# Optimization experiments

Measured on AMD Instinct MI355X. Metric: run time of the kernel, lower is better.

## Reference

```python
import jax, jax.numpy as jnp
import numpy as np

B, C, H, W = 16, 512, 64, 64
K = 32


def setup_inputs() -> dict:
    key = jax.random.key(0)
    k1, k2, k3 = jax.random.split(key, 3)
    std = 1.0 / (64 * C) ** 0.5
    x = jax.random.normal(k1, (B, C, H, W), dtype=jnp.float32)
    codewords = jax.random.uniform(k2, (K, C), dtype=jnp.float32, minval=-std, maxval=std)
    scale = jax.random.uniform(k3, (K,), dtype=jnp.float32, minval=-1.0, maxval=0.0)
    return {"x": x, "codewords": codewords, "scale": scale}


def reference(x, codewords, scale):
    b, c, h, w = x.shape
    # (b, n, c) with n = h*w spatial positions
    xf = x.reshape(b, c, h * w).transpose(0, 2, 1)
    x2 = jnp.sum(xf * xf, axis=-1)                       # (b, n)
    c2 = jnp.sum(codewords * codewords, axis=-1)          # (k,)
    xc = jnp.einsum('bnc,kc->bnk', xf, codewords)         # (b, n, k)
    logits = scale[None, None, :] * (x2[:, :, None] - 2.0 * xc + c2[None, None, :])
    A = jax.nn.softmax(logits, axis=2)                    # (b, n, k)
    # sum_n A[b,n,k] * (x[b,n,c] - codewords[k,c])
    encoded = jnp.einsum('bnk,bnc->bkc', A, xf) - jnp.einsum('bnk,kc->bkc', A, codewords)
    return encoded
```

## Files before the change

### kernel.cpp

```cpp
#include <hip/hip_runtime.h>
#include <hip/hip_bf16.h>
#include <math.h>

#define BB 16
#define CC 512
#define NN 4096
#define KK 32

typedef __attribute__((ext_vector_type(8))) short short8;
typedef __attribute__((ext_vector_type(4))) short short4v;
typedef __attribute__((ext_vector_type(4))) float float4v;

static __device__ __forceinline__ unsigned short f2bf(float f) {
  unsigned u = __float_as_uint(f);
  u += 0x7FFF + ((u >> 16) & 1);
  return (unsigned short)(u >> 16);
}

static __device__ __forceinline__ short8 cat8(short4v a, short4v b) {
  short8 r;
  r[0] = a[0]; r[1] = a[1]; r[2] = a[2]; r[3] = a[3];
  r[4] = b[0]; r[5] = b[1]; r[6] = b[2]; r[7] = b[3];
  return r;
}


__global__ __launch_bounds__(256) void prep_kernel(
    const float* __restrict__ cw, unsigned short* __restrict__ cwP,
    float* __restrict__ c2, float* __restrict__ asum) {
  int gid = blockIdx.x * 256 + threadIdx.x;
  if (gid < BB * KK) asum[gid] = 0.f;
  {
    int k = gid >> 9;
    int cc = gid & 511;
    int cs = cc & ~31;
    int w5 = cc & 31;
    int q = w5 >> 3, j = w5 & 7;
    int src_c = cs + 2 * q + (j & 1) + ((j >> 1) << 3);
    cwP[gid] = f2bf(cw[k * CC + src_c]);
  }
  __shared__ float c2p[KK][8];
  if (blockIdx.x == 0) {
    int k = threadIdx.x >> 3, j = threadIdx.x & 7;
    const float* row = cw + k * CC + j * 64;
    float s = 0.f;
    for (int i = 0; i < 64; ++i) s = fmaf(row[i], row[i], s);
    c2p[k][j] = s;
    __syncthreads();
    if (threadIdx.x < KK) {
      float t = 0.f;
      for (int j2 = 0; j2 < 8; ++j2) t += c2p[threadIdx.x][j2];
      c2[threadIdx.x] = t;
    }
  }
}

#define XP2 36
template <int LOG2CH>
__global__ __launch_bounds__(256, 4) void fused_kernel(
    const float* __restrict__ x, const unsigned short* __restrict__ cwP,
    const float* __restrict__ c2g, const float* __restrict__ scale,
    float* __restrict__ partials, float* __restrict__ asum) {
  constexpr int CHN = NN >> LOG2CH;
  constexpr int SUBS = CHN / 32;
  const int b = blockIdx.x >> LOG2CH;
  const int chunk = blockIdx.x & ((1 << LOG2CH) - 1);
  const int t = threadIdx.x;
  const int w = t >> 6;
  const int l = t & 63;
  const int l15 = l & 15;
  const int q = l >> 4;
  const int wrole = (w + (blockIdx.x & 3)) & 3;

  __shared__ unsigned short Xl[CC * XP2];
  __shared__ unsigned short As[KK * XP2];
  __shared__ float Sx2w[4 * 32];
  __shared__ float Sx2[32];

  const float* xb0 = x + (size_t)b * CC * NN + chunk * CHN;

  const float sc0 = scale[l15], sc1 = scale[16 + l15];
  const float cc0 = c2g[l15], cc1 = c2g[16 + l15];

  float4v acc[8][2];
#pragma unroll
  for (int ct = 0; ct < 8; ++ct)
#pragma unroll
    for (int m = 0; m < 2; ++m) acc[ct][m] = (float4v){0.f, 0.f, 0.f, 0.f};
  float s0acc = 0.f, s1acc = 0.f;

  const int f4 = t & 7;
  const int cr = t >> 3;

  for (int sub = 0; sub < SUBS; ++sub) {
    const float* xb = xb0 + sub * 32;

    float4v x2p = (float4v){0.f, 0.f, 0.f, 0.f};
#pragma unroll 8
    for (int i = 0; i < 16; ++i) {
      const int c = cr + 32 * i;
      float4v v = *(const float4v*)(xb + (size_t)c * NN + 4 * f4);
      x2p.x = fmaf(v.x, v.x, x2p.x);
      x2p.y = fmaf(v.y, v.y, x2p.y);
      x2p.z = fmaf(v.z, v.z, x2p.z);
      x2p.w = fmaf(v.w, v.w, x2p.w);
      unsigned p0 = (unsigned)f2bf(v.x) | ((unsigned)f2bf(v.y) << 16);
      unsigned p1 = (unsigned)f2bf(v.z) | ((unsigned)f2bf(v.w) << 16);
      *(uint2*)&Xl[c * XP2 + 4 * f4] = make_uint2(p0, p1);
    }
#pragma unroll
    for (int m = 8; m <= 32; m <<= 1) {
      x2p.x += __shfl_xor(x2p.x, m);
      x2p.y += __shfl_xor(x2p.y, m);
      x2p.z += __shfl_xor(x2p.z, m);
      x2p.w += __shfl_xor(x2p.w, m);
    }
    if (l < 8) *(float4v*)&Sx2w[w * 32 + 4 * l] = x2p;
    __syncthreads();

    float4v p0 = (float4v){0.f, 0.f, 0.f, 0.f};
    float4v p1 = (float4v){0.f, 0.f, 0.f, 0.f};
    if (wrole < 2) {
      const int nrow = wrole * 16 + l15;
      for (int cs = 0; cs < 512; cs += 32) {
        const int cb2 = cs + 2 * q;
        short8 af;
#pragma unroll
        for (int j = 0; j < 8; ++j) {
          const int c = cb2 + (j & 1) + ((j >> 1) << 3);
          af[j] = (short)Xl[c * XP2 + nrow];
        }
        short8 b0 = *(const short8*)(cwP + (size_t)l15 * CC + cs + q * 8);
        short8 b1 = *(const short8*)(cwP + (size_t)(16 + l15) * CC + cs + q * 8);
        p0 = __builtin_amdgcn_mfma_f32_16x16x32_bf16(af, b0, p0, 0, 0, 0);
        p1 = __builtin_amdgcn_mfma_f32_16x16x32_bf16(af, b1, p1, 0, 0, 0);
      }
    } else if (wrole == 2 && l < 32) {
      Sx2[l] = Sx2w[l] + Sx2w[32 + l] + Sx2w[64 + l] + Sx2w[96 + l];
    }
    __syncthreads();

    if (wrole < 2) {
      float a0[4], a1[4];
#pragma unroll
      for (int r = 0; r < 4; ++r) {
        const float xx = Sx2[wrole * 16 + 4 * q + r];
        float l0 = sc0 * (xx - 2.f * p0[r] + cc0);
        float l1 = sc1 * (xx - 2.f * p1[r] + cc1);
        float m = fmaxf(l0, l1);
        m = fmaxf(m, __shfl_xor(m, 1));
        m = fmaxf(m, __shfl_xor(m, 2));
        m = fmaxf(m, __shfl_xor(m, 4));
        m = fmaxf(m, __shfl_xor(m, 8));
        float e0 = __expf(l0 - m), e1 = __expf(l1 - m);
        float s = e0 + e1;
        s += __shfl_xor(s, 1);
        s += __shfl_xor(s, 2);
        s += __shfl_xor(s, 4);
        s += __shfl_xor(s, 8);
        float inv = 1.0f / s;
        a0[r] = e0 * inv;
        a1[r] = e1 * inv;
      }
      s0acc += a0[0] + a0[1] + a0[2] + a0[3];
      s1acc += a1[0] + a1[1] + a1[2] + a1[3];
      unsigned p00 = (unsigned)f2bf(a0[0]) | ((unsigned)f2bf(a0[1]) << 16);
      unsigned p01 = (unsigned)f2bf(a0[2]) | ((unsigned)f2bf(a0[3]) << 16);
      unsigned p10 = (unsigned)f2bf(a1[0]) | ((unsigned)f2bf(a1[1]) << 16);
      unsigned p11 = (unsigned)f2bf(a1[2]) | ((unsigned)f2bf(a1[3]) << 16);
      const int nc = wrole * 16 + 4 * q;
      *(uint2*)&As[l15 * XP2 + nc] = make_uint2(p00, p01);
      *(uint2*)&As[(16 + l15) * XP2 + nc] = make_uint2(p10, p11);
    }
    __syncthreads();

    {
      const int nb = q * 8;
      const short4v* Ap0 = (const short4v*)&As[l15 * XP2 + nb];
      const short4v* Ap1 = (const short4v*)&As[(16 + l15) * XP2 + nb];
      short8 am0 = cat8(Ap0[0], Ap0[1]);
      short8 am1 = cat8(Ap1[0], Ap1[1]);
#pragma unroll
      for (int ct = 0; ct < 8; ++ct) {
        const int c = w * 128 + ct * 16 + l15;
        const short4v* Bp = (const short4v*)&Xl[c * XP2 + nb];
        short8 bx = cat8(Bp[0], Bp[1]);
        acc[ct][0] = __builtin_amdgcn_mfma_f32_16x16x32_bf16(am0, bx, acc[ct][0], 0, 0, 0);
        acc[ct][1] = __builtin_amdgcn_mfma_f32_16x16x32_bf16(am1, bx, acc[ct][1], 0, 0, 0);
      }
    }
    __syncthreads();
  }

  float* pout = partials + (size_t)blockIdx.x * KK * CC;
#pragma unroll
  for (int ct = 0; ct < 8; ++ct) {
    const int c = w * 128 + ct * 16 + l15;
#pragma unroll
    for (int m = 0; m < 2; ++m)
#pragma unroll
      for (int r = 0; r < 4; ++r) {
        int k = 16 * m + 4 * q + r;
        pout[k * CC + c] = acc[ct][m][r];
      }
  }
  s0acc += __shfl_xor(s0acc, 16);
  s0acc += __shfl_xor(s0acc, 32);
  s1acc += __shfl_xor(s1acc, 16);
  s1acc += __shfl_xor(s1acc, 32);
  if (wrole < 2 && q == 0) {
    atomicAdd(&asum[b * KK + l15], s0acc);
    atomicAdd(&asum[b * KK + 16 + l15], s1acc);
  }
}

template <int LOG2CH>
__global__ __launch_bounds__(256) void reduce_kernel(
    const float* __restrict__ partials, const float* __restrict__ asum,
    const float* __restrict__ cw, float* __restrict__ out) {
  constexpr int P = 1 << LOG2CH;
  int idx = blockIdx.x * 256 + threadIdx.x;
  int b = idx >> 12;
  int k = (idx >> 7) & 31;
  int c4 = idx & 127;

  float4v o = {0.f, 0.f, 0.f, 0.f};
  const float4v* pb =
      (const float4v*)partials + (((size_t)b << LOG2CH) * KK + k) * 128 + c4;
#pragma unroll 8
  for (int p = 0; p < P; ++p) {
    float4v v = pb[(size_t)p * KK * 128];
    o.x += v.x;
    o.y += v.y;
    o.z += v.z;
    o.w += v.w;
  }
  float4v wv = ((const float4v*)cw)[k * 128 + c4];
  float a = asum[b * KK + k];
  o.x -= a * wv.x;
  o.y -= a * wv.y;
  o.z -= a * wv.z;
  o.w -= a * wv.w;
  ((float4v*)out)[idx] = o;
}

extern "C" void kernel_launch(void* const* d_in, const int* in_sizes, int n_in,
                              void* d_out, int out_size, void* d_ws, size_t ws_size,
                              hipStream_t stream) {
  const float* x = (const float*)d_in[0];
  const float* cw = (const float*)d_in[1];
  const float* scale = (const float*)d_in[2];
  float* out = (float*)d_out;
  char* ws = (char*)d_ws;

  float* c2 = (float*)ws;
  unsigned short* cwP = (unsigned short*)(ws + 128);
  float* asum = (float*)(ws + 32896);
  float* partials = (float*)(ws + 35072);

  prep_kernel<<<64, 256, 0, stream>>>(cw, cwP, c2, asum);

  const size_t need1024 = 35072 + (size_t)1024 * KK * CC * sizeof(float);
  if (ws_size >= need1024) {
    fused_kernel<6><<<1024, 256, 0, stream>>>(x, cwP, c2, scale, partials, asum);
    reduce_kernel<6><<<256, 256, 0, stream>>>(partials, asum, cw, out);
  } else {
    fused_kernel<5><<<512, 256, 0, stream>>>(x, cwP, c2, scale, partials, asum);
    reduce_kernel<5><<<256, 256, 0, stream>>>(partials, asum, cw, out);
  }
}
```

Before: 226.3 us.

## Prefetch next x sub-tile into registers and use LDS-only barriers

Software-pipelines the global loads of x: the first half of the next sub-tile's channels is loaded into registers while the current sub-tile's GEMM and softmax stages run, and the second half is issued at the start of each iteration. __syncthreads is replaced with a custom barrier that only waits on LDS counters, so outstanding global prefetch loads are not drained at each barrier. This hides HBM latency at the cost of extra VGPRs (two arrays of 8 float4s), which may lower occupancy.

Measured after the change: 272.8 us. 20.5% more time.

```diff
diff --git a/kernel.cpp b/kernel.cpp
--- a/kernel.cpp
+++ b/kernel.cpp
@@ -22,6 +22,11 @@
   r[0] = a[0]; r[1] = a[1]; r[2] = a[2]; r[3] = a[3];
   r[4] = b[0]; r[5] = b[1]; r[6] = b[2]; r[7] = b[3];
   return r;
+}
+
+static __device__ __forceinline__ void bar_lds() {
+  asm volatile("s_waitcnt lgkmcnt(0)" ::: "memory");
+  __builtin_amdgcn_s_barrier();
 }
 
 
@@ -92,14 +97,24 @@
   const int f4 = t & 7;
   const int cr = t >> 3;
 
+  float4v xr[8];
+#pragma unroll
+  for (int i = 0; i < 8; ++i)
+    xr[i] = *(const float4v*)(xb0 + (size_t)(cr + 32 * i) * NN + 4 * f4);
+
   for (int sub = 0; sub < SUBS; ++sub) {
     const float* xb = xb0 + sub * 32;
 
+    float4v xin[8];
+#pragma unroll
+    for (int i = 0; i < 8; ++i)
+      xin[i] = *(const float4v*)(xb + (size_t)(cr + 32 * (i + 8)) * NN + 4 * f4);
+
     float4v x2p = (float4v){0.f, 0.f, 0.f, 0.f};
-#pragma unroll 8
-    for (int i = 0; i < 16; ++i) {
+#pragma unroll
+    for (int i = 0; i < 8; ++i) {
       const int c = cr + 32 * i;
-      float4v v = *(const float4v*)(xb + (size_t)c * NN + 4 * f4);
+      float4v v = xr[i];
       x2p.x = fmaf(v.x, v.x, x2p.x);
       x2p.y = fmaf(v.y, v.y, x2p.y);
       x2p.z = fmaf(v.z, v.z, x2p.z);
@@ -109,6 +124,26 @@
       *(uint2*)&Xl[c * XP2 + 4 * f4] = make_uint2(p0, p1);
     }
 #pragma unroll
+    for (int i = 0; i < 8; ++i) {
+      const int c = cr + 32 * (i + 8);
+      float4v v = xin[i];
+      x2p.x = fmaf(v.x, v.x, x2p.x);
+      x2p.y = fmaf(v.y, v.y, x2p.y);
+      x2p.z = fmaf(v.z, v.z, x2p.z);
+      x2p.w = fmaf(v.w, v.w, x2p.w);
+      unsigned p0 = (unsigned)f2bf(v.x) | ((unsigned)f2bf(v.y) << 16);
+      unsigned p1 = (unsigned)f2bf(v.z) | ((unsigned)f2bf(v.w) << 16);
+      *(uint2*)&Xl[c * XP2 + 4 * f4] = make_uint2(p0, p1);
+    }
+
+    if (sub + 1 < SUBS) {
+      const float* xb2 = xb0 + (sub + 1) * 32;
+#pragma unroll
+      for (int i = 0; i < 8; ++i)
+        xr[i] = *(const float4v*)(xb2 + (size_t)(cr + 32 * i) * NN + 4 * f4);
+    }
+
+#pragma unroll
     for (int m = 8; m <= 32; m <<= 1) {
       x2p.x += __shfl_xor(x2p.x, m);
       x2p.y += __shfl_xor(x2p.y, m);
@@ -116,7 +151,7 @@
       x2p.w += __shfl_xor(x2p.w, m);
     }
     if (l < 8) *(float4v*)&Sx2w[w * 32 + 4 * l] = x2p;
-    __syncthreads();
+    bar_lds();
 
     float4v p0 = (float4v){0.f, 0.f, 0.f, 0.f};
     float4v p1 = (float4v){0.f, 0.f, 0.f, 0.f};
@@ -138,7 +173,7 @@
     } else if (wrole == 2 && l < 32) {
       Sx2[l] = Sx2w[l] + Sx2w[32 + l] + Sx2w[64 + l] + Sx2w[96 + l];
     }
-    __syncthreads();
+    bar_lds();
 
     if (wrole < 2) {
       float a0[4], a1[4];
@@ -172,7 +207,7 @@
       *(uint2*)&As[l15 * XP2 + nc] = make_uint2(p00, p01);
       *(uint2*)&As[(16 + l15) * XP2 + nc] = make_uint2(p10, p11);
     }
-    __syncthreads();
+    bar_lds();
 
     {
       const int nb = q * 8;
@@ -189,7 +224,7 @@
         acc[ct][1] = __builtin_amdgcn_mfma_f32_16x16x32_bf16(am1, bx, acc[ct][1], 0, 0, 0);
       }
     }
-    __syncthreads();
+    bar_lds();
   }
 
   float* pout = partials + (size_t)blockIdx.x * KK * CC;
```

## Pre-convert x to bf16 tiled layout and precompute squared norms in separate passes

Applied to the files above, without the earlier changes.

Adds a pass that reads x once, converts it to bf16 in a tile-contiguous layout, and writes partial squared norms. A small kernel then sums those norms. The fused kernel now loads contiguous bf16 tiles with 16-byte loads instead of strided fp32 rows, and reads precomputed x2 instead of reducing it. This is meant to remove strided global reads and conversion work from the MFMA kernel. In exchange it adds two extra launches and an extra write and read of a bf16 copy of x (about 64MB) plus partial norms. The old path is kept as a fallback when the workspace is too small.

After: 276.4 us. +22.1%, slower.

```diff
diff --git a/kernel.cpp b/kernel.cpp
--- a/kernel.cpp
+++ b/kernel.cpp
@@ -10,6 +10,7 @@
 typedef __attribute__((ext_vector_type(8))) short short8;
 typedef __attribute__((ext_vector_type(4))) short short4v;
 typedef __attribute__((ext_vector_type(4))) float float4v;
+typedef __attribute__((ext_vector_type(4))) unsigned int uint4v;
 
 static __device__ __forceinline__ unsigned short f2bf(float f) {
   unsigned u = __float_as_uint(f);
@@ -55,16 +56,62 @@
   }
 }
 
+__global__ __launch_bounds__(256) void passA_kernel(
+    const float* __restrict__ x, unsigned short* __restrict__ xt,
+    float* __restrict__ x2p) {
+  const int b = blockIdx.x >> 4;
+  const int slab = blockIdx.x & 15;
+  const int t = threadIdx.x;
+  const float* xb = x + (size_t)b * CC * NN + (size_t)slab * 32 * NN;
+
+  float4v x2a[4];
+#pragma unroll
+  for (int i = 0; i < 4; ++i) x2a[i] = (float4v){0.f, 0.f, 0.f, 0.f};
+
+  for (int cl = 0; cl < 32; ++cl) {
+    const float* row = xb + (size_t)cl * NN;
+    const int c = slab * 32 + cl;
+#pragma unroll
+    for (int i = 0; i < 4; ++i) {
+      const int n0 = i * 1024 + t * 4;
+      float4v v = *(const float4v*)(row + n0);
+      x2a[i].x = fmaf(v.x, v.x, x2a[i].x);
+      x2a[i].y = fmaf(v.y, v.y, x2a[i].y);
+      x2a[i].z = fmaf(v.z, v.z, x2a[i].z);
+      x2a[i].w = fmaf(v.w, v.w, x2a[i].w);
+      unsigned p0 = (unsigned)f2bf(v.x) | ((unsigned)f2bf(v.y) << 16);
+      unsigned p1 = (unsigned)f2bf(v.z) | ((unsigned)f2bf(v.w) << 16);
+      const int chunk = n0 >> 6;
+      const int sub = (n0 >> 5) & 1;
+      const int n32 = n0 & 31;
+      size_t off = ((((size_t)(b * 64 + chunk) * 2 + sub) * CC + c) * 32 + n32);
+      *(uint2*)&xt[off] = make_uint2(p0, p1);
+    }
+  }
+#pragma unroll
+  for (int i = 0; i < 4; ++i)
+    *(float4v*)&x2p[((size_t)(b * 16 + slab)) * NN + i * 1024 + t * 4] = x2a[i];
+}
+
+__global__ __launch_bounds__(256) void x2sum_kernel(
+    const float* __restrict__ x2p, float* __restrict__ x2f) {
+  int g = blockIdx.x * 256 + threadIdx.x;
+  int b = g >> 12;
+  int n = g & 4095;
+  float s = 0.f;
+#pragma unroll
+  for (int sl = 0; sl < 16; ++sl) s += x2p[((size_t)(b * 16 + sl)) * NN + n];
+  x2f[g] = s;
+}
+
 #define XP2 36
-template <int LOG2CH>
-__global__ __launch_bounds__(256, 4) void fused_kernel(
-    const float* __restrict__ x, const unsigned short* __restrict__ cwP,
-    const float* __restrict__ c2g, const float* __restrict__ scale,
-    float* __restrict__ partials, float* __restrict__ asum) {
-  constexpr int CHN = NN >> LOG2CH;
-  constexpr int SUBS = CHN / 32;
-  const int b = blockIdx.x >> LOG2CH;
-  const int chunk = blockIdx.x & ((1 << LOG2CH) - 1);
+__global__ __launch_bounds__(256, 4) void fused_kernel_v6(
+    const unsigned short* __restrict__ xt, const float* __restrict__ x2f,
+    const unsigned short* __restrict__ cwP, const float* __restrict__ c2g,
+    const float* __restrict__ scale, float* __restrict__ partials,
+    float* __restrict__ asum) {
+  const int b = blockIdx.x >> 6;
+  const int chunk = blockIdx.x & 63;
   const int t = threadIdx.x;
   const int w = t >> 6;
   const int l = t & 63;
@@ -74,10 +121,7 @@
 
   __shared__ unsigned short Xl[CC * XP2];
   __shared__ unsigned short As[KK * XP2];
-  __shared__ float Sx2w[4 * 32];
   __shared__ float Sx2[32];
-
-  const float* xb0 = x + (size_t)b * CC * NN + chunk * CHN;
 
   const float sc0 = scale[l15], sc1 = scale[16 + l15];
   const float cc0 = c2g[l15], cc1 = c2g[16 + l15];
@@ -89,33 +133,17 @@
     for (int m = 0; m < 2; ++m) acc[ct][m] = (float4v){0.f, 0.f, 0.f, 0.f};
   float s0acc = 0.f, s1acc = 0.f;
 
-  const int f4 = t & 7;
-  const int cr = t >> 3;
-
-  for (int sub = 0; sub < SUBS; ++sub) {
-    const float* xb = xb0 + sub * 32;
-
-    float4v x2p = (float4v){0.f, 0.f, 0.f, 0.f};
-#pragma unroll 8
-    for (int i = 0; i < 16; ++i) {
-      const int c = cr + 32 * i;
-      float4v v = *(const float4v*)(xb + (size_t)c * NN + 4 * f4);
-      x2p.x = fmaf(v.x, v.x, x2p.x);
-      x2p.y = fmaf(v.y, v.y, x2p.y);
-      x2p.z = fmaf(v.z, v.z, x2p.z);
-      x2p.w = fmaf(v.w, v.w, x2p.w);
-      unsigned p0 = (unsigned)f2bf(v.x) | ((unsigned)f2bf(v.y) << 16);
-      unsigned p1 = (unsigned)f2bf(v.z) | ((unsigned)f2bf(v.w) << 16);
-      *(uint2*)&Xl[c * XP2 + 4 * f4] = make_uint2(p0, p1);
-    }
-#pragma unroll
-    for (int m = 8; m <= 32; m <<= 1) {
-      x2p.x += __shfl_xor(x2p.x, m);
-      x2p.y += __shfl_xor(x2p.y, m);
-      x2p.z += __shfl_xor(x2p.z, m);
-      x2p.w += __shfl_xor(x2p.w, m);
-    }
-    if (l < 8) *(float4v*)&Sx2w[w * 32 + 4 * l] = x2p;
+  for (int sub = 0; sub < 2; ++sub) {
+    const unsigned short* tile = xt + ((size_t)(blockIdx.x * 2 + sub)) * (CC * 32);
+#pragma unroll
+    for (int i = 0; i < 8; ++i) {
+      const int idx = i * 256 + t;
+      const int c = idx >> 2;
+      const int f = idx & 3;
+      uint4v v = *(const uint4v*)(tile + (size_t)idx * 8);
+      *(uint2*)&Xl[c * XP2 + 8 * f] = make_uint2(v.x, v.y);
+      *(uint2*)&Xl[c * XP2 + 8 * f + 4] = make_uint2(v.z, v.w);
+    }
     __syncthreads();
 
     float4v p0 = (float4v){0.f, 0.f, 0.f, 0.f};
@@ -136,7 +164,7 @@
         p1 = __builtin_amdgcn_mfma_f32_16x16x32_bf16(af, b1, p1, 0, 0, 0);
       }
     } else if (wrole == 2 && l < 32) {
-      Sx2[l] = Sx2w[l] + Sx2w[32 + l] + Sx2w[64 + l] + Sx2w[96 + l];
+      Sx2[l] = x2f[b * NN + chunk * 64 + sub * 32 + l];
     }
     __syncthreads();
 
@@ -215,6 +243,162 @@
 }
 
 template <int LOG2CH>
+__global__ __launch_bounds__(256, 4) void fused_kernel_legacy(
+    const float* __restrict__ x, const unsigned short* __restrict__ cwP,
+    const float* __restrict__ c2g, const float* __restrict__ scale,
+    float* __restrict__ partials, float* __restrict__ asum) {
+  constexpr int CHN = NN >> LOG2CH;
+  constexpr int SUBS = CHN / 32;
+  const int b = blockIdx.x >> LOG2CH;
+  const int chunk = blockIdx.x & ((1 << LOG2CH) - 1);
+  const int t = threadIdx.x;
+  const int w = t >> 6;
+  const int l = t & 63;
+  const int l15 = l & 15;
+  const int q = l >> 4;
+  const int wrole = (w + (blockIdx.x & 3)) & 3;
+
+  __shared__ unsigned short Xl[CC * XP2];
+  __shared__ unsigned short As[KK * XP2];
+  __shared__ float Sx2w[4 * 32];
+  __shared__ float Sx2[32];
+
+  const float* xb0 = x + (size_t)b * CC * NN + chunk * CHN;
+  const float sc0 = scale[l15], sc1 = scale[16 + l15];
+  const float cc0 = c2g[l15], cc1 = c2g[16 + l15];
+
+  float4v acc[8][2];
+#pragma unroll
+  for (int ct = 0; ct < 8; ++ct)
+#pragma unroll
+    for (int m = 0; m < 2; ++m) acc[ct][m] = (float4v){0.f, 0.f, 0.f, 0.f};
+  float s0acc = 0.f, s1acc = 0.f;
+
+  const int f4 = t & 7;
+  const int cr = t >> 3;
+
+  for (int sub = 0; sub < SUBS; ++sub) {
+    const float* xb = xb0 + sub * 32;
+    float4v x2p = (float4v){0.f, 0.f, 0.f, 0.f};
+#pragma unroll 8
+    for (int i = 0; i < 16; ++i) {
+      const int c = cr + 32 * i;
+      float4v v = *(const float4v*)(xb + (size_t)c * NN + 4 * f4);
+      x2p.x = fmaf(v.x, v.x, x2p.x);
+      x2p.y = fmaf(v.y, v.y, x2p.y);
+      x2p.z = fmaf(v.z, v.z, x2p.z);
+      x2p.w = fmaf(v.w, v.w, x2p.w);
+      unsigned p0 = (unsigned)f2bf(v.x) | ((unsigned)f2bf(v.y) << 16);
+      unsigned p1 = (unsigned)f2bf(v.z) | ((unsigned)f2bf(v.w) << 16);
+      *(uint2*)&Xl[c * XP2 + 4 * f4] = make_uint2(p0, p1);
+    }
+#pragma unroll
+    for (int m = 8; m <= 32; m <<= 1) {
+      x2p.x += __shfl_xor(x2p.x, m);
+      x2p.y += __shfl_xor(x2p.y, m);
+      x2p.z += __shfl_xor(x2p.z, m);
+      x2p.w += __shfl_xor(x2p.w, m);
+    }
+    if (l < 8) *(float4v*)&Sx2w[w * 32 + 4 * l] = x2p;
+    __syncthreads();
+
+    float4v p0 = (float4v){0.f, 0.f, 0.f, 0.f};
+    float4v p1 = (float4v){0.f, 0.f, 0.f, 0.f};
+    if (wrole < 2) {
+      const int nrow = wrole * 16 + l15;
+      for (int cs = 0; cs < 512; cs += 32) {
+        const int cb2 = cs + 2 * q;
+        short8 af;
+#pragma unroll
+        for (int j = 0; j < 8; ++j) {
+          const int c = cb2 + (j & 1) + ((j >> 1) << 3);
+          af[j] = (short)Xl[c * XP2 + nrow];
+        }
+        short8 b0 = *(const short8*)(cwP + (size_t)l15 * CC + cs + q * 8);
+        short8 b1 = *(const short8*)(cwP + (size_t)(16 + l15) * CC + cs + q * 8);
+        p0 = __builtin_amdgcn_mfma_f32_16x16x32_bf16(af, b0, p0, 0, 0, 0);
+        p1 = __builtin_amdgcn_mfma_f32_16x16x32_bf16(af, b1, p1, 0, 0, 0);
+      }
+    } else if (wrole == 2 && l < 32) {
+      Sx2[l] = Sx2w[l] + Sx2w[32 + l] + Sx2w[64 + l] + Sx2w[96 + l];
+    }
+    __syncthreads();
+
+    if (wrole < 2) {
+      float a0[4], a1[4];
+#pragma unroll
+      for (int r = 0; r < 4; ++r) {
+        const float xx = Sx2[wrole * 16 + 4 * q + r];
+        float l0 = sc0 * (xx - 2.f * p0[r] + cc0);
+        float l1 = sc1 * (xx - 2.f * p1[r] + cc1);
+        float m = fmaxf(l0, l1);
+        m = fmaxf(m, __shfl_xor(m, 1));
+        m = fmaxf(m, __shfl_xor(m, 2));
+        m = fmaxf(m, __shfl_xor(m, 4));
+        m = fmaxf(m, __shfl_xor(m, 8));
+        float e0 = __expf(l0 - m), e1 = __expf(l1 - m);
+        float s = e0 + e1;
+        s += __shfl_xor(s, 1);
+        s += __shfl_xor(s, 2);
+        s += __shfl_xor(s, 4);
+        s += __shfl_xor(s, 8);
+        float inv = 1.0f / s;
+        a0[r] = e0 * inv;
+        a1[r] = e1 * inv;
+      }
+      s0acc += a0[0] + a0[1] + a0[2] + a0[3];
+      s1acc += a1[0] + a1[1] + a1[2] + a1[3];
+      unsigned p00 = (unsigned)f2bf(a0[0]) | ((unsigned)f2bf(a0[1]) << 16);
+      unsigned p01 = (unsigned)f2bf(a0[2]) | ((unsigned)f2bf(a0[3]) << 16);
+      unsigned p10 = (unsigned)f2bf(a1[0]) | ((unsigned)f2bf(a1[1]) << 16);
+      unsigned p11 = (unsigned)f2bf(a1[2]) | ((unsigned)f2bf(a1[3]) << 16);
+      const int nc = wrole * 16 + 4 * q;
+      *(uint2*)&As[l15 * XP2 + nc] = make_uint2(p00, p01);
+      *(uint2*)&As[(16 + l15) * XP2 + nc] = make_uint2(p10, p11);
+    }
+    __syncthreads();
+
+    {
+      const int nb = q * 8;
+      const short4v* Ap0 = (const short4v*)&As[l15 * XP2 + nb];
+      const short4v* Ap1 = (const short4v*)&As[(16 + l15) * XP2 + nb];
+      short8 am0 = cat8(Ap0[0], Ap0[1]);
+      short8 am1 = cat8(Ap1[0], Ap1[1]);
+#pragma unroll
+      for (int ct = 0; ct < 8; ++ct) {
+        const int c = w * 128 + ct * 16 + l15;
+        const short4v* Bp = (const short4v*)&Xl[c * XP2 + nb];
+        short8 bx = cat8(Bp[0], Bp[1]);
+        acc[ct][0] = __builtin_amdgcn_mfma_f32_16x16x32_bf16(am0, bx, acc[ct][0], 0, 0, 0);
+        acc[ct][1] = __builtin_amdgcn_mfma_f32_16x16x32_bf16(am1, bx, acc[ct][1], 0, 0, 0);
+      }
+    }
+    __syncthreads();
+  }
+
+  float* pout = partials + (size_t)blockIdx.x * KK * CC;
+#pragma unroll
+  for (int ct = 0; ct < 8; ++ct) {
+    const int c = w * 128 + ct * 16 + l15;
+#pragma unroll
+    for (int m = 0; m < 2; ++m)
+#pragma unroll
+      for (int r = 0; r < 4; ++r) {
+        int k = 16 * m + 4 * q + r;
+        pout[k * CC + c] = acc[ct][m][r];
+      }
+  }
+  s0acc += __shfl_xor(s0acc, 16);
+  s0acc += __shfl_xor(s0acc, 32);
+  s1acc += __shfl_xor(s1acc, 16);
+  s1acc += __shfl_xor(s1acc, 32);
+  if (wrole < 2 && q == 0) {
+    atomicAdd(&asum[b * KK + l15], s0acc);
+    atomicAdd(&asum[b * KK + 16 + l15], s1acc);
+  }
+}
+
+template <int LOG2CH>
 __global__ __launch_bounds__(256) void reduce_kernel(
     const float* __restrict__ partials, const float* __restrict__ asum,
     const float* __restrict__ cw, float* __restrict__ out) {
@@ -256,16 +440,33 @@
   float* c2 = (float*)ws;
   unsigned short* cwP = (unsigned short*)(ws + 128);
   float* asum = (float*)(ws + 32896);
-  float* partials = (float*)(ws + 35072);
+
+  constexpr size_t X2P_OFF = 35072;
+  constexpr size_t X2P_SZ = (size_t)BB * 16 * NN * 4;
+  constexpr size_t X2F_OFF = X2P_OFF + X2P_SZ;
+  constexpr size_t X2F_SZ = (size_t)BB * NN * 4;
+  constexpr size_t XT_OFF = X2F_OFF + X2F_SZ;
+  constexpr size_t XT_SZ = (size_t)BB * 64 * 2 * CC * 32 * 2;
+  constexpr size_t PART_OFF = XT_OFF + XT_SZ;
+  constexpr size_t PART_SZ = (size_t)1024 * KK * CC * 4;
+  constexpr size_t NEED = PART_OFF + PART_SZ;
 
   prep_kernel<<<64, 256, 0, stream>>>(cw, cwP, c2, asum);
 
-  const size_t need1024 = 35072 + (size_t)1024 * KK * CC * sizeof(float);
-  if (ws_size >= need1024) {
-    fused_kernel<6><<<1024, 256, 0, stream>>>(x, cwP, c2, scale, partials, asum);
+  if (ws_size >= NEED) {
+    float* x2p = (float*)(ws + X2P_OFF);
+    float* x2f = (float*)(ws + X2F_OFF);
+    unsigned short* xt = (unsigned short*)(ws + XT_OFF);
+    float* partials = (float*)(ws + PART_OFF);
+    passA_kernel<<<256, 256, 0, stream>>>(x, xt, x2p);
+    x2sum_kernel<<<256, 256, 0, stream>>>(x2p, x2f);
+    fused_kernel_v6<<<1024, 256, 0, stream>>>(xt, x2f, cwP, c2, scale,
+                                              partials, asum);
     reduce_kernel<6><<<256, 256, 0, stream>>>(partials, asum, cw, out);
   } else {
-    fused_kernel<5><<<512, 256, 0, stream>>>(x, cwP, c2, scale, partials, asum);
+    float* partials = (float*)(ws + 35072);
+    fused_kernel_legacy<5><<<512, 256, 0, stream>>>(x, cwP, c2, scale,
+                                                    partials, asum);
     reduce_kernel<5><<<256, 256, 0, stream>>>(partials, asum, cw, out);
   }
 }
```
